# Performance work log

Hardware: AMD Instinct MI355X
Metric: run time of the kernel (lower is better)

Reference implementation:

```python
import jax, jax.numpy as jnp
import numpy as np

B, IN_DIM, K, D = 8192, 1024, 2048, 256
TAU = 1.0
BN_EPS = 1e-5


def setup_inputs() -> dict:
    key = jax.random.key(0)
    ks = jax.random.split(key, 4)
    x = jax.random.normal(ks[0], (B, IN_DIM), dtype=jnp.float32)
    u = jax.random.uniform(ks[1], (B, K), dtype=jnp.float32)  # uniform for gumbel noise
    W = jax.random.normal(ks[2], (IN_DIM, D), dtype=jnp.float32) * 0.02
    b = jnp.zeros((D,), dtype=jnp.float32)
    gamma = jnp.ones((D,), dtype=jnp.float32)
    beta = jnp.zeros((D,), dtype=jnp.float32)
    E = jax.random.normal(ks[3], (K, D), dtype=jnp.float32)  # nn.Embedding default N(0,1)
    return {"x": x, "u": u, "W": W, "b": b, "gamma": gamma, "beta": beta, "E": E}


def reference(x, u, W, b, gamma, beta, E):
    # classifier + BatchNorm1d (training mode: batch stats, biased variance)
    h = x @ W + b                                   # [B, D]
    mu = jnp.mean(h, axis=0)
    var = jnp.var(h, axis=0)
    h = (h - mu) * jax.lax.rsqrt(var + BN_EPS) * gamma + beta
    # negative squared euclidean distance via ||h||^2 - 2 h.E^T + ||e||^2 (GEMM form,
    # avoids materializing [B, K, D])
    h2 = jnp.sum(h * h, axis=-1, keepdims=True)     # [B, 1]
    e2 = jnp.sum(E * E, axis=-1)                    # [K]
    logits = -(h2 - 2.0 * (h @ E.T) + e2)           # [B, K]
    # gumbel-softmax (soft) with tau
    g = -jnp.log(-jnp.log(u + 1e-10) + 1e-10)
    assignments = jax.nn.softmax((logits + g) / TAU, axis=-1)  # [B, K]
    z = assignments @ E                             # [B, D]
    probs = jax.nn.softmax(logits, axis=-1)
    return probs, z
```

## Files before the change

### kernel.cpp

```cpp
#include <hip/hip_runtime.h>
#include <math.h>

#define B_SZ 8192
#define IN_DIM 1024
#define K_CB 2048
#define D_SZ 256
#define BN_EPS 1e-5f

typedef _Float16 f16;
typedef _Float16 f16x8 __attribute__((ext_vector_type(8)));
typedef _Float16 f16x4 __attribute__((ext_vector_type(4)));
typedef float    f32x4 __attribute__((ext_vector_type(4)));

#define GLOAD_LDS16(g, l) __builtin_amdgcn_global_load_lds(                      \
    (const __attribute__((address_space(1))) unsigned int*)(g),                  \
    (__attribute__((address_space(3))) unsigned int*)(l), 16, 0, 0)

template<int BM, int BN, int BK, int EPI, bool A32>
__global__ __launch_bounds__(256) void gemm_mfma(
    const void* __restrict__ Aptr, int lda,
    const f16* __restrict__ Bptr, int ldb,
    void* __restrict__ Cptr, int ldc, int Kdim,
    const float* __restrict__ bias, const float* __restrict__ h2v,
    const float* __restrict__ e2v)
{
    constexpr int G    = BK / 8;
    constexpr int MASK = G - 1;
    constexpr int WM = BM / 2, WN = BN / 2;
    constexpr int FM = WM / 16, FN = WN / 16;
    constexpr int CH_A = BM * G;
    constexpr int CH_B = BN * G;

    __shared__ char lds[(BM + BN) * BK * 2];
    char* As = lds;
    char* Bs = lds + BM * BK * 2;

    const int tid  = threadIdx.x;
    const int w    = tid >> 6, lane = tid & 63;
    const int wm   = w >> 1,   wn   = w & 1;
    const int row0 = blockIdx.x * BM;
    const int col0 = blockIdx.y * BN;

    f32x4 acc[FM][FN] = {};

    for (int k0 = 0; k0 < Kdim; k0 += BK) {
        #pragma unroll
        for (int i = 0; i < CH_B / 256; ++i) {
            const int base = (i * 4 + w) * 64;
            const int s = base + lane;
            const int r = s / G, c = s % G;
            const f16* src = Bptr + (size_t)(col0 + r) * ldb + k0 + ((c ^ (r & MASK)) * 8);
            GLOAD_LDS16(src, Bs + base * 16);
        }
        if (!A32) {
            #pragma unroll
            for (int i = 0; i < CH_A / 256; ++i) {
                const int base = (i * 4 + w) * 64;
                const int s = base + lane;
                const int r = s / G, c = s % G;
                const f16* src = (const f16*)Aptr + (size_t)(row0 + r) * lda + k0 + ((c ^ (r & MASK)) * 8);
                GLOAD_LDS16(src, As + base * 16);
            }
        } else {
            #pragma unroll
            for (int i = 0; i < CH_A / 256; ++i) {
                const int s = i * 256 + tid;
                const int r = s / G, c = s % G;
                const float* src = (const float*)Aptr + (size_t)(row0 + r) * lda + k0 + c * 8;
                const float4 v0 = ((const float4*)src)[0];
                const float4 v1 = ((const float4*)src)[1];
                f16x8 d;
                d[0] = (f16)v0.x; d[1] = (f16)v0.y; d[2] = (f16)v0.z; d[3] = (f16)v0.w;
                d[4] = (f16)v1.x; d[5] = (f16)v1.y; d[6] = (f16)v1.z; d[7] = (f16)v1.w;
                *(f16x8*)(As + (r * G + (c ^ (r & MASK))) * 16) = d;
            }
        }
        __syncthreads();

        #pragma unroll
        for (int kk = 0; kk < BK / 32; ++kk) {
            f16x8 af[FM], bf[FN];
            #pragma unroll
            for (int m = 0; m < FM; ++m) {
                const int r = wm * WM + m * 16 + (lane & 15);
                const int g = (kk * 4 + (lane >> 4)) ^ (r & MASK);
                af[m] = *(const f16x8*)(As + r * (BK * 2) + g * 16);
            }
            #pragma unroll
            for (int n = 0; n < FN; ++n) {
                const int r = wn * WN + n * 16 + (lane & 15);
                const int g = (kk * 4 + (lane >> 4)) ^ (r & MASK);
                bf[n] = *(const f16x8*)(Bs + r * (BK * 2) + g * 16);
            }
            #pragma unroll
            for (int m = 0; m < FM; ++m)
                #pragma unroll
                for (int n = 0; n < FN; ++n)
                    acc[m][n] = __builtin_amdgcn_mfma_f32_16x16x32_f16(af[m], bf[n], acc[m][n], 0, 0, 0);
        }
        __syncthreads();
    }

    #pragma unroll
    for (int m = 0; m < FM; ++m) {
        const int rbase = row0 + wm * WM + m * 16 + (lane >> 4) * 4;
        #pragma unroll
        for (int n = 0; n < FN; ++n) {
            const int c = col0 + wn * WN + n * 16 + (lane & 15);
            #pragma unroll
            for (int j = 0; j < 4; ++j) {
                const float v = acc[m][n][j];
                if (EPI == 0) {
                    ((float*)Cptr)[(size_t)(rbase + j) * ldc + c] = v;
                } else if (EPI == 1) {
                    ((f16*)Cptr)[(size_t)(rbase + j) * ldc + c] = (f16)(v + bias[c]);
                } else {
                    ((float*)Cptr)[(size_t)(rbase + j) * ldc + c] =
                        2.0f * v - h2v[rbase + j] - e2v[c];
                }
            }
        }
    }
}

__global__ __launch_bounds__(256) void conv_WT(const float* __restrict__ W, f16* __restrict__ WT)
{
    const int r = blockIdx.x, c = threadIdx.x;
    WT[c * 1024 + r] = (f16)W[r * 256 + c];
}

__global__ __launch_bounds__(256) void conv_E(const float* __restrict__ E,
                                              f16* __restrict__ E16, f16* __restrict__ ET)
{
    const int r = blockIdx.x, c = threadIdx.x;
    const float v = E[r * 256 + c];
    E16[r * 256 + c] = (f16)v;
    ET[c * 2048 + r] = (f16)v;
}

__global__ __launch_bounds__(256) void bn_partial(const f16* __restrict__ h16, float* __restrict__ part)
{
    const int d = threadIdx.x;
    const int blk = blockIdx.x;
    const int r0 = blk * (B_SZ / 128);
    float s = 0.f, sq = 0.f;
    for (int r = r0; r < r0 + (B_SZ / 128); ++r) {
        const float v = (float)h16[(size_t)r * D_SZ + d];
        s += v; sq += v * v;
    }
    part[blk * 512 + d]       = s;
    part[blk * 512 + 256 + d] = sq;
}

__global__ __launch_bounds__(256) void bn_finalize(
    const float* __restrict__ part, const float* __restrict__ gamma, const float* __restrict__ beta,
    float* __restrict__ scale, float* __restrict__ shift)
{
    const int d = threadIdx.x;
    float s = 0.f, sq = 0.f;
    for (int b = 0; b < 128; ++b) { s += part[b * 512 + d]; sq += part[b * 512 + 256 + d]; }
    const float mu  = s / (float)B_SZ;
    const float var = sq / (float)B_SZ - mu * mu;
    const float sc  = gamma[d] * rsqrtf(var + BN_EPS);
    scale[d] = sc;
    shift[d] = beta[d] - mu * sc;
}

__global__ __launch_bounds__(256) void norm_h2(
    f16* __restrict__ h16, const float* __restrict__ scale, const float* __restrict__ shift,
    float* __restrict__ h2out)
{
    const int wave = threadIdx.x >> 6, lane = threadIdx.x & 63;
    const int row = blockIdx.x * 4 + wave;
    f16x4* hp = (f16x4*)(h16 + (size_t)row * D_SZ);
    f16x4 v = hp[lane];
    const float4 sc = ((const float4*)scale)[lane];
    const float4 sh = ((const float4*)shift)[lane];
    const float f0 = fmaf((float)v[0], sc.x, sh.x);
    const float f1 = fmaf((float)v[1], sc.y, sh.y);
    const float f2 = fmaf((float)v[2], sc.z, sh.z);
    const float f3 = fmaf((float)v[3], sc.w, sh.w);
    v[0] = (f16)f0; v[1] = (f16)f1; v[2] = (f16)f2; v[3] = (f16)f3;
    hp[lane] = v;
    float ss = f0 * f0 + f1 * f1 + f2 * f2 + f3 * f3;
    #pragma unroll
    for (int off = 32; off > 0; off >>= 1) ss += __shfl_down(ss, off);
    if (lane == 0) h2out[row] = ss;
}

__global__ __launch_bounds__(256) void e2_kernel(const float* __restrict__ E, float* __restrict__ e2)
{
    const int wave = threadIdx.x >> 6, lane = threadIdx.x & 63;
    const int row = blockIdx.x * 4 + wave;
    const float4 v = ((const float4*)(E + (size_t)row * D_SZ))[lane];
    float ss = v.x * v.x + v.y * v.y + v.z * v.z + v.w * v.w;
    #pragma unroll
    for (int off = 32; off > 0; off >>= 1) ss += __shfl_down(ss, off);
    if (lane == 0) e2[row] = ss;
}

__global__ __launch_bounds__(256) void softmax_dual(
    const float* __restrict__ logits, const float* __restrict__ u,
    float* __restrict__ probs, f16* __restrict__ assign16)
{
    const int row = blockIdx.x;
    const int tid = threadIdx.x;
    const int wave = tid >> 6, lane = tid & 63;
    __shared__ float red[2][4];

    const float4* L4 = (const float4*)(logits + (size_t)row * K_CB);
    const float4* U4 = (const float4*)(u + (size_t)row * K_CB);
    const float4 la = L4[tid * 2], lb = L4[tid * 2 + 1];
    const float4 ua = U4[tid * 2], ub = U4[tid * 2 + 1];
    float l[8]  = {la.x, la.y, la.z, la.w, lb.x, lb.y, lb.z, lb.w};
    float uu[8] = {ua.x, ua.y, ua.z, ua.w, ub.x, ub.y, ub.z, ub.w};
    float s2[8];
    float m1 = -1e30f, m2 = -1e30f;
    #pragma unroll
    for (int j = 0; j < 8; ++j) {
        const float g = -logf(-logf(uu[j] + 1e-10f) + 1e-10f);
        s2[j] = l[j] + g;
        m1 = fmaxf(m1, l[j]);
        m2 = fmaxf(m2, s2[j]);
    }
    #pragma unroll
    for (int off = 32; off > 0; off >>= 1) {
        m1 = fmaxf(m1, __shfl_down(m1, off));
        m2 = fmaxf(m2, __shfl_down(m2, off));
    }
    if (lane == 0) { red[0][wave] = m1; red[1][wave] = m2; }
    __syncthreads();
    m1 = fmaxf(fmaxf(red[0][0], red[0][1]), fmaxf(red[0][2], red[0][3]));
    m2 = fmaxf(fmaxf(red[1][0], red[1][1]), fmaxf(red[1][2], red[1][3]));
    __syncthreads();

    float p1[8], p2[8];
    float sum1 = 0.f, sum2 = 0.f;
    #pragma unroll
    for (int j = 0; j < 8; ++j) {
        p1[j] = expf(l[j]  - m1); sum1 += p1[j];
        p2[j] = expf(s2[j] - m2); sum2 += p2[j];
    }
    #pragma unroll
    for (int off = 32; off > 0; off >>= 1) {
        sum1 += __shfl_down(sum1, off);
        sum2 += __shfl_down(sum2, off);
    }
    if (lane == 0) { red[0][wave] = sum1; red[1][wave] = sum2; }
    __syncthreads();
    const float r1 = 1.f / (red[0][0] + red[0][1] + red[0][2] + red[0][3]);
    const float r2 = 1.f / (red[1][0] + red[1][1] + red[1][2] + red[1][3]);

    float4* P4 = (float4*)(probs + (size_t)row * K_CB);
    float4 o;
    o = make_float4(p1[0] * r1, p1[1] * r1, p1[2] * r1, p1[3] * r1); P4[tid * 2]     = o;
    o = make_float4(p1[4] * r1, p1[5] * r1, p1[6] * r1, p1[7] * r1); P4[tid * 2 + 1] = o;

    f16* A16 = assign16 + (size_t)row * 4096;
    f16x8 a8;
    #pragma unroll
    for (int j = 0; j < 8; ++j) a8[j] = (f16)(p2[j] * r2);
    *(f16x8*)(A16 + tid * 8) = a8;
}

extern "C" void kernel_launch(void* const* d_in, const int* in_sizes, int n_in,
                              void* d_out, int out_size, void* d_ws, size_t ws_size,
                              hipStream_t stream)
{
    const float* x     = (const float*)d_in[0];
    const float* u     = (const float*)d_in[1];
    const float* W     = (const float*)d_in[2];
    const float* bias  = (const float*)d_in[3];
    const float* gamma = (const float*)d_in[4];
    const float* beta  = (const float*)d_in[5];
    const float* E     = (const float*)d_in[6];

    float* probs = (float*)d_out;
    float* z     = probs + (size_t)B_SZ * K_CB;

    char* ws = (char*)d_ws;
    float* logits = (float*)ws;
    ws += (size_t)B_SZ * K_CB * 4;
    f16* h16 = (f16*)ws;      ws += (size_t)B_SZ * D_SZ * 2;
    f16* WT16 = (f16*)ws;     ws += (size_t)D_SZ * IN_DIM * 2;
    f16* E16 = (f16*)ws;      ws += (size_t)K_CB * D_SZ * 2;
    f16* ET16 = (f16*)ws;     ws += (size_t)D_SZ * K_CB * 2;
    float* part = (float*)ws; ws += 128 * 512 * 4;
    float* scale = (float*)ws; ws += D_SZ * 4;
    float* shift = (float*)ws; ws += D_SZ * 4;
    float* h2 = (float*)ws;   ws += B_SZ * 4;
    float* e2 = (float*)ws;   ws += K_CB * 4;
    f16* assign16 = (f16*)logits;

    conv_WT<<<IN_DIM, 256, 0, stream>>>(W, WT16);
    conv_E<<<K_CB, 256, 0, stream>>>(E, E16, ET16);
    e2_kernel<<<K_CB / 4, 256, 0, stream>>>(E, e2);

    {
        dim3 g(B_SZ / 64, D_SZ / 64);
        gemm_mfma<64, 64, 64, 1, true><<<g, 256, 0, stream>>>(
            x, IN_DIM, WT16, IN_DIM, h16, D_SZ, IN_DIM, bias, nullptr, nullptr);
    }
    bn_partial<<<128, 256, 0, stream>>>(h16, part);
    bn_finalize<<<1, 256, 0, stream>>>(part, gamma, beta, scale, shift);
    norm_h2<<<B_SZ / 4, 256, 0, stream>>>(h16, scale, shift, h2);

    {
        dim3 g(B_SZ / 128, K_CB / 128);
        gemm_mfma<128, 128, 64, 2, false><<<g, 256, 0, stream>>>(
            h16, D_SZ, E16, D_SZ, logits, K_CB, D_SZ, nullptr, h2, e2);
    }
    softmax_dual<<<B_SZ, 256, 0, stream>>>(logits, u, probs, assign16);

    {
        dim3 g(B_SZ / 64, D_SZ / 64);
        gemm_mfma<64, 64, 128, 0, false><<<g, 256, 0, stream>>>(
            assign16, 4096, ET16, K_CB, z, D_SZ, K_CB, nullptr, nullptr, nullptr);
    }
}
```

Before: 125.0 us.

## Fuse logits GEMM with dual softmax in one kernel, drop h2 term

Replaces the separate logits GEMM and row-softmax kernels with a single kernel. Each block computes a 32-row by 2048-column logits strip in registers, streams E through double-buffered swizzled LDS, computes the Gumbel noise inline, and writes probs and fp16 assignments directly. This removes the fp32 logits round-trip through HBM. It also drops the per-row ||h||^2 term, which cancels in softmax, and folds the e2 computation into the E conversion kernel. In exchange, the kernel holds a very large register footprint (32 accumulator tiles plus the Gumbel values) and launches only 256 blocks, which may limit occupancy and parallelism.

```diff
diff --git a/kernel.cpp b/kernel.cpp
--- a/kernel.cpp
+++ b/kernel.cpp
@@ -21,8 +21,7 @@
     const void* __restrict__ Aptr, int lda,
     const f16* __restrict__ Bptr, int ldb,
     void* __restrict__ Cptr, int ldc, int Kdim,
-    const float* __restrict__ bias, const float* __restrict__ h2v,
-    const float* __restrict__ e2v)
+    const float* __restrict__ bias)
 {
     constexpr int G    = BK / 8;
     constexpr int MASK = G - 1;
@@ -112,13 +111,153 @@
                 const float v = acc[m][n][j];
                 if (EPI == 0) {
                     ((float*)Cptr)[(size_t)(rbase + j) * ldc + c] = v;
-                } else if (EPI == 1) {
+                } else {
                     ((f16*)Cptr)[(size_t)(rbase + j) * ldc + c] = (f16)(v + bias[c]);
-                } else {
-                    ((float*)Cptr)[(size_t)(rbase + j) * ldc + c] =
-                        2.0f * v - h2v[rbase + j] - e2v[c];
                 }
             }
+        }
+    }
+}
+
+__global__ __launch_bounds__(512, 2) void fused_sm(
+    const f16* __restrict__ h16, const f16* __restrict__ E16,
+    const float* __restrict__ e2v, const float* __restrict__ u,
+    float* __restrict__ probs, f16* __restrict__ assign16)
+{
+    __shared__ f16 Bs[2][64 * 256];
+    __shared__ float redA[8][16], redB[8][16], redC[8][16], redD[8][16];
+
+    const int tid  = threadIdx.x;
+    const int w    = tid >> 6, lane = tid & 63;
+    const int q    = lane >> 4, r16 = lane & 15;
+    const int wc   = w & 3, wr = w >> 2;
+    const int row0 = blockIdx.x * 32;
+    const int colL = wc * 16 + r16;
+    const int rowA = row0 + wr * 16;
+
+    f16x8 af[8];
+    {
+        const f16* hrow = h16 + (size_t)(rowA + r16) * D_SZ + q * 8;
+        #pragma unroll
+        for (int kk = 0; kk < 8; ++kk) af[kk] = *(const f16x8*)(hrow + kk * 32);
+    }
+
+    f32x4 acc[32];
+    #pragma unroll
+    for (int n = 0; n < 32; ++n) acc[n] = (f32x4){0.f, 0.f, 0.f, 0.f};
+    f16x4 gv[32];
+
+    #pragma unroll
+    for (int i = 0; i < 4; ++i) {
+        const int base = i * 512 + w * 64;
+        const int s = base + lane;
+        const int r = s >> 5, cg = s & 31;
+        GLOAD_LDS16(E16 + (size_t)r * D_SZ + ((cg ^ (r & 31)) * 8), (f16*)Bs[0] + base * 8);
+    }
+    __syncthreads();
+
+    #pragma unroll
+    for (int c = 0; c < 32; ++c) {
+        const int buf = c & 1;
+        if (c < 31) {
+            #pragma unroll
+            for (int i = 0; i < 4; ++i) {
+                const int base = i * 512 + w * 64;
+                const int s = base + lane;
+                const int r = s >> 5, cg = s & 31;
+                GLOAD_LDS16(E16 + (size_t)((c + 1) * 64 + r) * D_SZ + ((cg ^ (r & 31)) * 8),
+                            (f16*)Bs[buf ^ 1] + base * 8);
+            }
+        }
+        {
+            const int col = c * 64 + colL;
+            const float* up = u + (size_t)(rowA + q * 4) * K_CB + col;
+            #pragma unroll
+            for (int j = 0; j < 4; ++j) {
+                const float uu = up[(size_t)j * K_CB];
+                gv[c][j] = (f16)(-__logf(-__logf(uu + 1e-10f) + 1e-10f));
+            }
+        }
+        #pragma unroll
+        for (int kk = 0; kk < 8; ++kk) {
+            const int gb = (kk * 4 + q) ^ (colL & 31);
+            const f16x8 bf = *(const f16x8*)((const f16*)Bs[buf] + colL * 256 + gb * 8);
+            acc[c] = __builtin_amdgcn_mfma_f32_16x16x32_f16(af[kk], bf, acc[c], 0, 0, 0);
+        }
+        __syncthreads();
+    }
+
+    float m1[4] = {-1e30f, -1e30f, -1e30f, -1e30f};
+    float m2[4] = {-1e30f, -1e30f, -1e30f, -1e30f};
+    #pragma unroll
+    for (int n = 0; n < 32; ++n) {
+        const float ec = e2v[n * 64 + colL];
+        #pragma unroll
+        for (int j = 0; j < 4; ++j) {
+            const float lv = 2.f * acc[n][j] - ec;
+            acc[n][j] = lv;
+            m1[j] = fmaxf(m1[j], lv);
+            m2[j] = fmaxf(m2[j], lv + (float)gv[n][j]);
+        }
+    }
+    #pragma unroll
+    for (int off = 1; off < 16; off <<= 1)
+        #pragma unroll
+        for (int j = 0; j < 4; ++j) {
+            m1[j] = fmaxf(m1[j], __shfl_xor(m1[j], off));
+            m2[j] = fmaxf(m2[j], __shfl_xor(m2[j], off));
+        }
+    if (r16 == 0)
+        #pragma unroll
+        for (int j = 0; j < 4; ++j) { redA[w][q * 4 + j] = m1[j]; redB[w][q * 4 + j] = m2[j]; }
+    __syncthreads();
+    #pragma unroll
+    for (int j = 0; j < 4; ++j) {
+        m1[j] = fmaxf(fmaxf(redA[wr * 4 + 0][q * 4 + j], redA[wr * 4 + 1][q * 4 + j]),
+                      fmaxf(redA[wr * 4 + 2][q * 4 + j], redA[wr * 4 + 3][q * 4 + j]));
+        m2[j] = fmaxf(fmaxf(redB[wr * 4 + 0][q * 4 + j], redB[wr * 4 + 1][q * 4 + j]),
+                      fmaxf(redB[wr * 4 + 2][q * 4 + j], redB[wr * 4 + 3][q * 4 + j]));
+    }
+
+    float s1[4] = {0.f, 0.f, 0.f, 0.f}, s2[4] = {0.f, 0.f, 0.f, 0.f};
+    #pragma unroll
+    for (int n = 0; n < 32; ++n)
+        #pragma unroll
+        for (int j = 0; j < 4; ++j) {
+            const float lv = acc[n][j];
+            const float e1 = __expf(lv - m1[j]);
+            const float eg = __expf(lv + (float)gv[n][j] - m2[j]);
+            acc[n][j] = e1; gv[n][j] = (f16)eg;
+            s1[j] += e1; s2[j] += eg;
+        }
+    #pragma unroll
+    for (int off = 1; off < 16; off <<= 1)
+        #pragma unroll
+        for (int j = 0; j < 4; ++j) {
+            s1[j] += __shfl_xor(s1[j], off);
+            s2[j] += __shfl_xor(s2[j], off);
+        }
+    if (r16 == 0)
+        #pragma unroll
+        for (int j = 0; j < 4; ++j) { redC[w][q * 4 + j] = s1[j]; redD[w][q * 4 + j] = s2[j]; }
+    __syncthreads();
+    float r1[4], r2[4];
+    #pragma unroll
+    for (int j = 0; j < 4; ++j) {
+        r1[j] = 1.f / (redC[wr * 4 + 0][q * 4 + j] + redC[wr * 4 + 1][q * 4 + j] +
+                       redC[wr * 4 + 2][q * 4 + j] + redC[wr * 4 + 3][q * 4 + j]);
+        r2[j] = 1.f / (redD[wr * 4 + 0][q * 4 + j] + redD[wr * 4 + 1][q * 4 + j] +
+                       redD[wr * 4 + 2][q * 4 + j] + redD[wr * 4 + 3][q * 4 + j]);
+    }
+
+    #pragma unroll
+    for (int n = 0; n < 32; ++n) {
+        const int col = n * 64 + colL;
+        #pragma unroll
+        for (int j = 0; j < 4; ++j) {
+            const int row = rowA + q * 4 + j;
+            probs[(size_t)row * K_CB + col] = acc[n][j] * r1[j];
+            assign16[(size_t)row * K_CB + col] = (f16)((float)gv[n][j] * r2[j]);
         }
     }
 }
@@ -129,13 +268,22 @@
     WT[c * 1024 + r] = (f16)W[r * 256 + c];
 }
 
-__global__ __launch_bounds__(256) void conv_E(const float* __restrict__ E,
-                                              f16* __restrict__ E16, f16* __restrict__ ET)
+__global__ __launch_bounds__(256) void conv_E2(const float* __restrict__ E,
+                                               f16* __restrict__ E16, f16* __restrict__ ET,
+                                               float* __restrict__ e2)
 {
     const int r = blockIdx.x, c = threadIdx.x;
+    const int wave = c >> 6, lane = c & 63;
     const float v = E[r * 256 + c];
     E16[r * 256 + c] = (f16)v;
     ET[c * 2048 + r] = (f16)v;
+    float ss = v * v;
+    #pragma unroll
+    for (int off = 32; off > 0; off >>= 1) ss += __shfl_down(ss, off);
+    __shared__ float s4[4];
+    if (lane == 0) s4[wave] = ss;
+    __syncthreads();
+    if (c == 0) e2[r] = s4[0] + s4[1] + s4[2] + s4[3];
 }
 
 __global__ __launch_bounds__(256) void bn_partial(const f16* __restrict__ h16, float* __restrict__ part)
@@ -166,9 +314,8 @@
     shift[d] = beta[d] - mu * sc;
 }
 
-__global__ __launch_bounds__(256) void norm_h2(
-    f16* __restrict__ h16, const float* __restrict__ scale, const float* __restrict__ shift,
-    float* __restrict__ h2out)
+__global__ __launch_bounds__(256) void norm_h(
+    f16* __restrict__ h16, const float* __restrict__ scale, const float* __restrict__ shift)
 {
     const int wave = threadIdx.x >> 6, lane = threadIdx.x & 63;
     const int row = blockIdx.x * 4 + wave;
@@ -176,91 +323,11 @@
     f16x4 v = hp[lane];
     const float4 sc = ((const float4*)scale)[lane];
     const float4 sh = ((const float4*)shift)[lane];
-    const float f0 = fmaf((float)v[0], sc.x, sh.x);
-    const float f1 = fmaf((float)v[1], sc.y, sh.y);
-    const float f2 = fmaf((float)v[2], sc.z, sh.z);
-    const float f3 = fmaf((float)v[3], sc.w, sh.w);
-    v[0] = (f16)f0; v[1] = (f16)f1; v[2] = (f16)f2; v[3] = (f16)f3;
+    v[0] = (f16)fmaf((float)v[0], sc.x, sh.x);
+    v[1] = (f16)fmaf((float)v[1], sc.y, sh.y);
+    v[2] = (f16)fmaf((float)v[2], sc.z, sh.z);
+    v[3] = (f16)fmaf((float)v[3], sc.w, sh.w);
     hp[lane] = v;
-    float ss = f0 * f0 + f1 * f1 + f2 * f2 + f3 * f3;
-    #pragma unroll
-    for (int off = 32; off > 0; off >>= 1) ss += __shfl_down(ss, off);
-    if (lane == 0) h2out[row] = ss;
-}
-
-__global__ __launch_bounds__(256) void e2_kernel(const float* __restrict__ E, float* __restrict__ e2)
-{
-    const int wave = threadIdx.x >> 6, lane = threadIdx.x & 63;
-    const int row = blockIdx.x * 4 + wave;
-    const float4 v = ((const float4*)(E + (size_t)row * D_SZ))[lane];
-    float ss = v.x * v.x + v.y * v.y + v.z * v.z + v.w * v.w;
-    #pragma unroll
-    for (int off = 32; off > 0; off >>= 1) ss += __shfl_down(ss, off);
-    if (lane == 0) e2[row] = ss;
-}
-
-__global__ __launch_bounds__(256) void softmax_dual(
-    const float* __restrict__ logits, const float* __restrict__ u,
-    float* __restrict__ probs, f16* __restrict__ assign16)
-{
-    const int row = blockIdx.x;
-    const int tid = threadIdx.x;
-    const int wave = tid >> 6, lane = tid & 63;
-    __shared__ float red[2][4];
-
-    const float4* L4 = (const float4*)(logits + (size_t)row * K_CB);
-    const float4* U4 = (const float4*)(u + (size_t)row * K_CB);
-    const float4 la = L4[tid * 2], lb = L4[tid * 2 + 1];
-    const float4 ua = U4[tid * 2], ub = U4[tid * 2 + 1];
-    float l[8]  = {la.x, la.y, la.z, la.w, lb.x, lb.y, lb.z, lb.w};
-    float uu[8] = {ua.x, ua.y, ua.z, ua.w, ub.x, ub.y, ub.z, ub.w};
-    float s2[8];
-    float m1 = -1e30f, m2 = -1e30f;
-    #pragma unroll
-    for (int j = 0; j < 8; ++j) {
-        const float g = -logf(-logf(uu[j] + 1e-10f) + 1e-10f);
-        s2[j] = l[j] + g;
-        m1 = fmaxf(m1, l[j]);
-        m2 = fmaxf(m2, s2[j]);
-    }
-    #pragma unroll
-    for (int off = 32; off > 0; off >>= 1) {
-        m1 = fmaxf(m1, __shfl_down(m1, off));
-        m2 = fmaxf(m2, __shfl_down(m2, off));
-    }
-    if (lane == 0) { red[0][wave] = m1; red[1][wave] = m2; }
-    __syncthreads();
-    m1 = fmaxf(fmaxf(red[0][0], red[0][1]), fmaxf(red[0][2], red[0][3]));
-    m2 = fmaxf(fmaxf(red[1][0], red[1][1]), fmaxf(red[1][2], red[1][3]));
-    __syncthreads();
-
-    float p1[8], p2[8];
-    float sum1 = 0.f, sum2 = 0.f;
-    #pragma unroll
-    for (int j = 0; j < 8; ++j) {
-        p1[j] = expf(l[j]  - m1); sum1 += p1[j];
-        p2[j] = expf(s2[j] - m2); sum2 += p2[j];
-    }
-    #pragma unroll
-    for (int off = 32; off > 0; off >>= 1) {
-        sum1 += __shfl_down(sum1, off);
-        sum2 += __shfl_down(sum2, off);
-    }
-    if (lane == 0) { red[0][wave] = sum1; red[1][wave] = sum2; }
-    __syncthreads();
-    const float r1 = 1.f / (red[0][0] + red[0][1] + red[0][2] + red[0][3]);
-    const float r2 = 1.f / (red[1][0] + red[1][1] + red[1][2] + red[1][3]);
-
-    float4* P4 = (float4*)(probs + (size_t)row * K_CB);
-    float4 o;
-    o = make_float4(p1[0] * r1, p1[1] * r1, p1[2] * r1, p1[3] * r1); P4[tid * 2]     = o;
-    o = make_float4(p1[4] * r1, p1[5] * r1, p1[6] * r1, p1[7] * r1); P4[tid * 2 + 1] = o;
-
-    f16* A16 = assign16 + (size_t)row * 4096;
-    f16x8 a8;
-    #pragma unroll
-    for (int j = 0; j < 8; ++j) a8[j] = (f16)(p2[j] * r2);
-    *(f16x8*)(A16 + tid * 8) = a8;
 }
 
 extern "C" void kernel_launch(void* const* d_in, const int* in_sizes, int n_in,
@@ -279,42 +346,33 @@
     float* z     = probs + (size_t)B_SZ * K_CB;
 
     char* ws = (char*)d_ws;
-    float* logits = (float*)ws;
-    ws += (size_t)B_SZ * K_CB * 4;
-    f16* h16 = (f16*)ws;      ws += (size_t)B_SZ * D_SZ * 2;
-    f16* WT16 = (f16*)ws;     ws += (size_t)D_SZ * IN_DIM * 2;
-    f16* E16 = (f16*)ws;      ws += (size_t)K_CB * D_SZ * 2;
-    f16* ET16 = (f16*)ws;     ws += (size_t)D_SZ * K_CB * 2;
-    float* part = (float*)ws; ws += 128 * 512 * 4;
+    f16* assign16 = (f16*)ws;  ws += (size_t)B_SZ * K_CB * 2;
+    f16* h16 = (f16*)ws;       ws += (size_t)B_SZ * D_SZ * 2;
+    f16* WT16 = (f16*)ws;      ws += (size_t)D_SZ * IN_DIM * 2;
+    f16* E16 = (f16*)ws;       ws += (size_t)K_CB * D_SZ * 2;
+    f16* ET16 = (f16*)ws;      ws += (size_t)D_SZ * K_CB * 2;
+    float* part = (float*)ws;  ws += 128 * 512 * 4;
     float* scale = (float*)ws; ws += D_SZ * 4;
     float* shift = (float*)ws; ws += D_SZ * 4;
-    float* h2 = (float*)ws;   ws += B_SZ * 4;
-    float* e2 = (float*)ws;   ws += K_CB * 4;
-    f16* assign16 = (f16*)logits;
+    float* e2 = (float*)ws;    ws += K_CB * 4;
 
     conv_WT<<<IN_DIM, 256, 0, stream>>>(W, WT16);
-    conv_E<<<K_CB, 256, 0, stream>>>(E, E16, ET16);
-    e2_kernel<<<K_CB / 4, 256, 0, stream>>>(E, e2);
+    conv_E2<<<K_CB, 256, 0, stream>>>(E, E16, ET16, e2);
 
     {
         dim3 g(B_SZ / 64, D_SZ / 64);
         gemm_mfma<64, 64, 64, 1, true><<<g, 256, 0, stream>>>(
-            x, IN_DIM, WT16, IN_DIM, h16, D_SZ, IN_DIM, bias, nullptr, nullptr);
+            x, IN_DIM, WT16, IN_DIM, h16, D_SZ, IN_DIM, bias);
     }
     bn_partial<<<128, 256, 0, stream>>>(h16, part);
     bn_finalize<<<1, 256, 0, stream>>>(part, gamma, beta, scale, shift);
-    norm_h2<<<B_SZ / 4, 256, 0, stream>>>(h16, scale, shift, h2);
-
-    {
-        dim3 g(B_SZ / 128, K_CB / 128);
-        gemm_mfma<128, 128, 64, 2, false><<<g, 256, 0, stream>>>(
-            h16, D_SZ, E16, D_SZ, logits, K_CB, D_SZ, nullptr, h2, e2);
-    }
-    softmax_dual<<<B_SZ, 256, 0, stream>>>(logits, u, probs, assign16);
+    norm_h<<<B_SZ / 4, 256, 0, stream>>>(h16, scale, shift);
+
+    fused_sm<<<B_SZ / 32, 512, 0, stream>>>(h16, E16, e2, u, probs, assign16);
 
     {
         dim3 g(B_SZ / 64, D_SZ / 64);
         gemm_mfma<64, 64, 128, 0, false><<<g, 256, 0, stream>>>(
-            assign16, 4096, ET16, K_CB, z, D_SZ, K_CB, nullptr, nullptr, nullptr);
-    }
-}
+            assign16, K_CB, ET16, K_CB, z, D_SZ, K_CB, nullptr);
+    }
+}
```

Result: slower. 238.3 us (+90.5%).
